# Kernel optimization log

Measured on AMD Instinct MI355X. Metric: run time of the kernel, lower is better.

The kernel has to match this reference:

```python
import jax, jax.numpy as jnp
import numpy as np

TOP_K = 8
NUM_EXPERTS = 256
HIDDEN = 7168
NUM_TOKENS = 16384
NORM_TOPK_PROB = True


def setup_inputs() -> dict:
    key = jax.random.key(0)
    k1, k2 = jax.random.split(key)
    hidden_states = jax.random.normal(k1, (NUM_TOKENS, HIDDEN), dtype=jnp.float32)
    weight = jax.random.normal(k2, (NUM_EXPERTS, HIDDEN), dtype=jnp.float32) * 0.02
    return {"hidden_states": hidden_states, "weight": weight}


def reference(hidden_states, weight):
    # Router logits: [T, E] = [T, H] @ [E, H]^T
    logits = jnp.einsum("th,eh->te", hidden_states, weight)
    # Fused softmax + top-k (npu_moe_gating_top_k_softmax semantics):
    # softmax over experts, then take top-k probabilities and their indices.
    probs = jax.nn.softmax(logits, axis=-1)
    topk_weight, topk_idx = jax.lax.top_k(probs, TOP_K)  # [T, k]
    # row_idx: expert-major (column-major) flattened row indices, as the NPU op returns.
    T = logits.shape[0]
    row_idx = jnp.arange(T * TOP_K, dtype=jnp.int32).reshape(TOP_K, T).T  # [T, k]
    if TOP_K > 1 and NORM_TOPK_PROB:
        denominator = jnp.sum(topk_weight, axis=-1, keepdims=True) + 1e-20
        topk_weight = topk_weight / denominator
    topk_idx = topk_idx.astype(jnp.int32)
    return (topk_idx, topk_weight, row_idx)
```

## Files before the change

kernel.cpp:

```cpp
#include <hip/hip_runtime.h>
#include <hip/hip_bf16.h>

#define NTOK 16384
#define HID 7168
#define NEXP 256
#define TOPK 8

typedef __bf16 bf16x8 __attribute__((ext_vector_type(8)));
typedef float  f32x16 __attribute__((ext_vector_type(16)));

__device__ __align__(16) unsigned short g_wb[NEXP * HID];

__device__ __forceinline__ unsigned int f2bfb(float x) {
    unsigned int u = __float_as_uint(x);
    return (u + 0x7fffu + ((u >> 16) & 1u)) >> 16;
}
__device__ __forceinline__ uint4 pk4(float4 p, float4 q) {
    uint4 u;
    u.x = f2bfb(p.x) | (f2bfb(p.y) << 16);
    u.y = f2bfb(p.z) | (f2bfb(p.w) << 16);
    u.z = f2bfb(q.x) | (f2bfb(q.y) << 16);
    u.w = f2bfb(q.z) | (f2bfb(q.w) << 16);
    return u;
}
__device__ __forceinline__ bf16x8 asbf8(uint4 u) {
    union { uint4 a; bf16x8 b; } c; c.a = u; return c.b;
}

__global__ void wconv_frag(const float* __restrict__ wt) {
    const int tid = blockIdx.x * 256 + threadIdx.x;
    const int l  = tid & 63;
    const int ks = (tid >> 6) & 7;
    const int g  = (tid >> 9) & 7;
    const int p  = tid >> 12;
    const int e  = g * 32 + (l & 31);
    const int kb = p * 128 + ks * 16 + ((l >> 5) << 3);
    const float4* s = (const float4*)(wt + (size_t)e * HID + kb);
    ((uint4*)g_wb)[tid] = pk4(s[0], s[1]);
}

__global__ void moe_rows(float* __restrict__ ob) {
    const int q = blockIdx.x * 256 + threadIdx.x;
    ob[262144 + q] = (float)((q & 7) * NTOK + (q >> 3));
}

__global__ __launch_bounds__(256, 2) void moe_gate_v16(
    const float* __restrict__ hs,
    float* __restrict__ ob)
{
    __shared__ __align__(16) char smem[65536];

    const int tid   = threadIdx.x;
    const int lane  = tid & 63;
    const int w     = tid >> 6;
    const int khalf = lane >> 5;
    const int t0    = blockIdx.x * 32;

    const int srow = tid >> 3;
    const int ssub = tid & 7;
    const char* astage = (const char*)(hs + (size_t)(t0 + srow) * HID + ssub * 8);
    const int stBase = srow * 2048 + ((ssub * 16) ^ ((srow & 7) << 4));

    const int arow  = lane & 31;
    const int abase = arow * 2048;
    const int aswz  = (arow & 7) << 4;

    const char* const bbase = (const char*)g_wb + (size_t)(w * 2) * 8192 + lane * 16;

    f32x16 acc0 = {}, acc1 = {};
    uint4 b0a, b0b, b1a, b1b, b2a, b2b, b3a, b3b;

#define ISSUE_B(SA, SB, J)                                                    \
    do {                                                                      \
        const char* bp = bbase + ((size_t)((J) >> 3) * 64 + ((J) & 7)) * 1024;\
        SA = *(const uint4*)(bp);                                             \
        SB = *(const uint4*)(bp + 8192);                                      \
        __builtin_amdgcn_sched_barrier(0);                                    \
    } while (0)

#define COMPUTE(JL, SA, SB)                                                   \
    do {                                                                      \
        const int off = (((JL) * 32 + khalf * 16) ^ aswz);                    \
        bf16x8 a = *(const bf16x8*)(smem + abase + off);                      \
        acc0 = __builtin_amdgcn_mfma_f32_32x32x16_bf16(a, asbf8(SA), acc0, 0, 0, 0); \
        acc1 = __builtin_amdgcn_mfma_f32_32x32x16_bf16(a, asbf8(SB), acc1, 0, 0, 0); \
    } while (0)

#define VMW(N)                                                                \
    do {                                                                      \
        asm volatile("s_waitcnt vmcnt(" #N ")" ::: "memory");                 \
        __builtin_amdgcn_sched_barrier(0);                                    \
    } while (0)

    for (int c = 0; c < 7; ++c) {
        __syncthreads();
        #pragma unroll
        for (int i = 0; i < 16; ++i) {
            float4 v0 = *(const float4*)(astage + (size_t)c * 4096 + i * 256);
            float4 v1 = *(const float4*)(astage + (size_t)c * 4096 + i * 256 + 16);
            *(uint4*)(smem + stBase + i * 128) = pk4(v0, v1);
        }
        __syncthreads();

        const int C64 = c * 64;
        ISSUE_B(b0a, b0b, C64 + 0);
        ISSUE_B(b1a, b1b, C64 + 1);
        ISSUE_B(b2a, b2b, C64 + 2);
        ISSUE_B(b3a, b3b, C64 + 3);

        for (int jj = 0; jj < 15; ++jj) {
            const int j = jj * 4;
            VMW(6); COMPUTE(j + 0, b0a, b0b); ISSUE_B(b0a, b0b, C64 + j + 4);
            VMW(6); COMPUTE(j + 1, b1a, b1b); ISSUE_B(b1a, b1b, C64 + j + 5);
            VMW(6); COMPUTE(j + 2, b2a, b2b); ISSUE_B(b2a, b2b, C64 + j + 6);
            VMW(6); COMPUTE(j + 3, b3a, b3b); ISSUE_B(b3a, b3b, C64 + j + 7);
        }
        VMW(6); COMPUTE(60, b0a, b0b);
        VMW(4); COMPUTE(61, b1a, b1b);
        VMW(2); COMPUTE(62, b2a, b2b);
        VMW(0); COMPUTE(63, b3a, b3b);
    }

    __syncthreads();

    float* ll = (float*)smem;
    {
        const int ec = w * 64 + (lane & 31);
        #pragma unroll
        for (int r = 0; r < 16; ++r) {
            const int tok = (r & 3) + 8 * (r >> 2) + 4 * khalf;
            ll[tok * 257 + ec]      = acc0[r];
            ll[tok * 257 + ec + 32] = acc1[r];
        }
    }
    __syncthreads();

    if (tid < 32) {
        const float* lr = ll + tid * 257;
        float bv[TOPK]; int bi8[TOPK];
        #pragma unroll
        for (int k = 0; k < TOPK; ++k) { bv[k] = -1e30f; bi8[k] = 0; }
        for (int e = 0; e < NEXP; ++e) {
            const float v = lr[e];
            if (v > bv[TOPK - 1]) {
                int k = TOPK - 1;
                while (k > 0 && v > bv[k - 1]) {
                    bv[k] = bv[k - 1]; bi8[k] = bi8[k - 1]; --k;
                }
                bv[k] = v; bi8[k] = e;
            }
        }
        float ev[TOPK], ssum = 0.f;
        #pragma unroll
        for (int r = 0; r < TOPK; ++r) { ev[r] = expf(bv[r] - bv[0]); ssum += ev[r]; }
        const float inv = 1.0f / ssum;

        const int tg = t0 + tid;
        #pragma unroll
        for (int r = 0; r < TOPK; ++r) {
            ob[(size_t)tg * TOPK + r]          = (float)bi8[r];
            ob[131072 + (size_t)tg * TOPK + r] = ev[r] * inv;
        }
    }
#undef ISSUE_B
#undef COMPUTE
#undef VMW
}

extern "C" void kernel_launch(void* const* d_in, const int* in_sizes, int n_in,
                              void* d_out, int out_size, void* d_ws, size_t ws_size,
                              hipStream_t stream) {
    const float* hs = (const float*)d_in[0];
    const float* wt = (const float*)d_in[1];
    float* ob = (float*)d_out;

    wconv_frag<<<dim3(NEXP * HID / 8 / 256), dim3(256), 0, stream>>>(wt);
    moe_gate_v16<<<dim3(NTOK / 32), dim3(256), 0, stream>>>(hs, ob);
    moe_rows<<<dim3(512), dim3(256), 0, stream>>>(ob);
}
```

Baseline: 245.5 us.

## Split experts across 8 waves, halve K-chunk, stagger chunk order per block

The gating GEMM kernel now uses 512 threads (8 waves), each owning 32 experts with a single accumulator instead of 4 waves with 64 experts each. The K loop stages 512-element chunks (half the shared memory), so more blocks can be resident. It also deepens B prefetch to 8 registers, remaps block IDs to tokens, and rotates each block's starting chunk so concurrent blocks read different weight regions. The intent is better occupancy, latency hiding and spread-out L2/HBM traffic, at the cost of twice as many barrier-separated staging phases.

```diff
diff --git a/kernel.cpp b/kernel.cpp
--- a/kernel.cpp
+++ b/kernel.cpp
@@ -5,6 +5,8 @@
 #define HID 7168
 #define NEXP 256
 #define TOPK 8
+#define NCHK 14
+#define CSTEP 32
 
 typedef __bf16 bf16x8 __attribute__((ext_vector_type(8)));
 typedef float  f32x16 __attribute__((ext_vector_type(16)));
@@ -44,93 +46,100 @@
     ob[262144 + q] = (float)((q & 7) * NTOK + (q >> 3));
 }
 
-__global__ __launch_bounds__(256, 2) void moe_gate_v16(
+__global__ __launch_bounds__(512, 4) void moe_gate_v17(
     const float* __restrict__ hs,
     float* __restrict__ ob)
 {
-    __shared__ __align__(16) char smem[65536];
+    __shared__ __align__(16) char smem[33792];
 
     const int tid   = threadIdx.x;
     const int lane  = tid & 63;
     const int w     = tid >> 6;
     const int khalf = lane >> 5;
-    const int t0    = blockIdx.x * 32;
+    const int bid   = blockIdx.x;
+    const int sb    = (bid & 7) * 64 + (bid >> 3);
+    const int t0    = sb * 32;
+    const int boff  = bid % NCHK;
 
-    const int srow = tid >> 3;
-    const int ssub = tid & 7;
-    const char* astage = (const char*)(hs + (size_t)(t0 + srow) * HID + ssub * 8);
-    const int stBase = srow * 2048 + ((ssub * 16) ^ ((srow & 7) << 4));
+    const int srow = tid >> 4;
+    const int ssub = tid & 15;
+    const float* astage = hs + (size_t)(t0 + srow) * HID + ssub * 32;
+    int adst[4];
+    #pragma unroll
+    for (int d = 0; d < 4; ++d)
+        adst[d] = srow * 1024 + (((ssub * 4 + d) ^ (srow & 7)) << 4);
 
     const int arow  = lane & 31;
-    const int abase = arow * 2048;
-    const int aswz  = (arow & 7) << 4;
+    const int abase = arow * 1024;
+    const int amask = arow & 7;
 
-    const char* const bbase = (const char*)g_wb + (size_t)(w * 2) * 8192 + lane * 16;
+    const char* const bbase = (const char*)g_wb + w * 8192 + lane * 16;
 
-    f32x16 acc0 = {}, acc1 = {};
-    uint4 b0a, b0b, b1a, b1b, b2a, b2b, b3a, b3b;
+    f32x16 acc = {};
+    uint4 b0, b1, b2, b3, b4, b5, b6, b7;
 
-#define ISSUE_B(SA, SB, J)                                                    \
+#define BADDR(J16) (bbase + (size_t)(((J16) >> 3) * 64 + ((J16) & 7)) * 1024)
+#define LOADB(R, J16)                                                         \
+    do { R = *(const uint4*)BADDR(J16); __builtin_amdgcn_sched_barrier(0); } while (0)
+#define CMP(J, R)                                                             \
     do {                                                                      \
-        const char* bp = bbase + ((size_t)((J) >> 3) * 64 + ((J) & 7)) * 1024;\
-        SA = *(const uint4*)(bp);                                             \
-        SB = *(const uint4*)(bp + 8192);                                      \
-        __builtin_amdgcn_sched_barrier(0);                                    \
+        const int off = ((((J) * 2 + khalf) ^ amask) << 4);                   \
+        bf16x8 a = *(const bf16x8*)(smem + abase + off);                      \
+        acc = __builtin_amdgcn_mfma_f32_32x32x16_bf16(a, asbf8(R), acc, 0, 0, 0); \
     } while (0)
-
-#define COMPUTE(JL, SA, SB)                                                   \
-    do {                                                                      \
-        const int off = (((JL) * 32 + khalf * 16) ^ aswz);                    \
-        bf16x8 a = *(const bf16x8*)(smem + abase + off);                      \
-        acc0 = __builtin_amdgcn_mfma_f32_32x32x16_bf16(a, asbf8(SA), acc0, 0, 0, 0); \
-        acc1 = __builtin_amdgcn_mfma_f32_32x32x16_bf16(a, asbf8(SB), acc1, 0, 0, 0); \
-    } while (0)
-
 #define VMW(N)                                                                \
     do {                                                                      \
         asm volatile("s_waitcnt vmcnt(" #N ")" ::: "memory");                 \
         __builtin_amdgcn_sched_barrier(0);                                    \
     } while (0)
 
-    for (int c = 0; c < 7; ++c) {
+    for (int c = 0; c < NCHK; ++c) {
+        int cc = c + boff; if (cc >= NCHK) cc -= NCHK;
+
         __syncthreads();
         #pragma unroll
-        for (int i = 0; i < 16; ++i) {
-            float4 v0 = *(const float4*)(astage + (size_t)c * 4096 + i * 256);
-            float4 v1 = *(const float4*)(astage + (size_t)c * 4096 + i * 256 + 16);
-            *(uint4*)(smem + stBase + i * 128) = pk4(v0, v1);
+        for (int d = 0; d < 4; ++d) {
+            float4 v0 = *(const float4*)(astage + (size_t)cc * 512 + d * 8);
+            float4 v1 = *(const float4*)(astage + (size_t)cc * 512 + d * 8 + 4);
+            *(uint4*)(smem + adst[d]) = pk4(v0, v1);
         }
         __syncthreads();
 
-        const int C64 = c * 64;
-        ISSUE_B(b0a, b0b, C64 + 0);
-        ISSUE_B(b1a, b1b, C64 + 1);
-        ISSUE_B(b2a, b2b, C64 + 2);
-        ISSUE_B(b3a, b3b, C64 + 3);
+        const int J0 = cc * CSTEP;
+        LOADB(b0, J0 + 0); LOADB(b1, J0 + 1); LOADB(b2, J0 + 2); LOADB(b3, J0 + 3);
+        LOADB(b4, J0 + 4); LOADB(b5, J0 + 5); LOADB(b6, J0 + 6); LOADB(b7, J0 + 7);
 
-        for (int jj = 0; jj < 15; ++jj) {
-            const int j = jj * 4;
-            VMW(6); COMPUTE(j + 0, b0a, b0b); ISSUE_B(b0a, b0b, C64 + j + 4);
-            VMW(6); COMPUTE(j + 1, b1a, b1b); ISSUE_B(b1a, b1b, C64 + j + 5);
-            VMW(6); COMPUTE(j + 2, b2a, b2b); ISSUE_B(b2a, b2b, C64 + j + 6);
-            VMW(6); COMPUTE(j + 3, b3a, b3b); ISSUE_B(b3a, b3b, C64 + j + 7);
+        #pragma unroll
+        for (int jj = 0; jj < 3; ++jj) {
+            const int j = jj * 8;
+            VMW(7); CMP(j + 0, b0); LOADB(b0, J0 + j +  8);
+            VMW(7); CMP(j + 1, b1); LOADB(b1, J0 + j +  9);
+            VMW(7); CMP(j + 2, b2); LOADB(b2, J0 + j + 10);
+            VMW(7); CMP(j + 3, b3); LOADB(b3, J0 + j + 11);
+            VMW(7); CMP(j + 4, b4); LOADB(b4, J0 + j + 12);
+            VMW(7); CMP(j + 5, b5); LOADB(b5, J0 + j + 13);
+            VMW(7); CMP(j + 6, b6); LOADB(b6, J0 + j + 14);
+            VMW(7); CMP(j + 7, b7); LOADB(b7, J0 + j + 15);
         }
-        VMW(6); COMPUTE(60, b0a, b0b);
-        VMW(4); COMPUTE(61, b1a, b1b);
-        VMW(2); COMPUTE(62, b2a, b2b);
-        VMW(0); COMPUTE(63, b3a, b3b);
+        VMW(7); CMP(24, b0);
+        VMW(6); CMP(25, b1);
+        VMW(5); CMP(26, b2);
+        VMW(4); CMP(27, b3);
+        VMW(3); CMP(28, b4);
+        VMW(2); CMP(29, b5);
+        VMW(1); CMP(30, b6);
+        VMW(0); CMP(31, b7);
     }
 
     __syncthreads();
 
     float* ll = (float*)smem;
     {
-        const int ec = w * 64 + (lane & 31);
+        const int ec = w * 32 + (lane & 31);
         #pragma unroll
         for (int r = 0; r < 16; ++r) {
             const int tok = (r & 3) + 8 * (r >> 2) + 4 * khalf;
-            ll[tok * 257 + ec]      = acc0[r];
-            ll[tok * 257 + ec + 32] = acc1[r];
+            ll[tok * 257 + ec] = acc[r];
         }
     }
     __syncthreads();
@@ -162,8 +171,9 @@
             ob[131072 + (size_t)tg * TOPK + r] = ev[r] * inv;
         }
     }
-#undef ISSUE_B
-#undef COMPUTE
+#undef BADDR
+#undef LOADB
+#undef CMP
 #undef VMW
 }
 
@@ -175,6 +185,6 @@
     float* ob = (float*)d_out;
 
     wconv_frag<<<dim3(NEXP * HID / 8 / 256), dim3(256), 0, stream>>>(wt);
-    moe_gate_v16<<<dim3(NTOK / 32), dim3(256), 0, stream>>>(hs, ob);
+    moe_gate_v17<<<dim3(NTOK / 32), dim3(512), 0, stream>>>(hs, ob);
     moe_rows<<<dim3(512), dim3(256), 0, stream>>>(ob);
 }
```

After: 264.7 us. 1.08x slower.

## Use 256-token tiles with split-K partials and a separate top-k reduce kernel

Applied to the files above, without the earlier changes.

The gating GEMM now runs as 512-thread blocks that each own 256 tokens and a quarter of the hidden dimension, so there are 64x4 blocks. This replaces 512 blocks of 32 tokens that each streamed the whole bf16 weight matrix. Weight tiles are copied straight into LDS with global_load_lds and double-buffered alongside the converted activation tiles. Each block writes fp32 partial logits to the workspace, and a new reduce kernel sums the splits and does the top-k softmax. This should cut repeated weight traffic from L2 and keep the matrix cores busier, at the cost of extra workspace reads and writes and one more kernel launch.

```diff
diff --git a/kernel.cpp b/kernel.cpp
--- a/kernel.cpp
+++ b/kernel.cpp
@@ -8,6 +8,8 @@
 
 typedef __bf16 bf16x8 __attribute__((ext_vector_type(8)));
 typedef float  f32x16 __attribute__((ext_vector_type(16)));
+typedef __attribute__((address_space(1))) const unsigned char ga_t;
+typedef __attribute__((address_space(3))) unsigned char la_t;
 
 __device__ __align__(16) unsigned short g_wb[NEXP * HID];
 
@@ -23,8 +25,8 @@
     u.w = f2bfb(q.z) | (f2bfb(q.w) << 16);
     return u;
 }
-__device__ __forceinline__ bf16x8 asbf8(uint4 u) {
-    union { uint4 a; bf16x8 b; } c; c.a = u; return c.b;
+__device__ __forceinline__ void gll16(const void* g, void* l) {
+    __builtin_amdgcn_global_load_lds((ga_t*)g, (la_t*)l, 16, 0, 0);
 }
 
 __global__ void wconv_frag(const float* __restrict__ wt) {
@@ -44,98 +46,182 @@
     ob[262144 + q] = (float)((q & 7) * NTOK + (q >> 3));
 }
 
-__global__ __launch_bounds__(256, 2) void moe_gate_v16(
+template<int KS>
+__global__ __launch_bounds__(512, 1) void moe_gate_v19(
     const float* __restrict__ hs,
+    float* __restrict__ pw)
+{
+    constexpr int KLEN  = HID / KS;
+    constexpr int NSTEP = KLEN / 64;
+    __shared__ __align__(16) char smem[131072];
+    char* const bA0 = smem;
+    char* const bA1 = smem + 32768;
+    char* const bB0 = smem + 65536;
+    char* const bB1 = smem + 98304;
+
+    const int tid   = threadIdx.x;
+    const int lane  = tid & 63;
+    const int l31   = lane & 31;
+    const int khalf = lane >> 5;
+    const int wv    = tid >> 6;
+    const int wm    = wv >> 2;
+    const int wn    = wv & 3;
+    const int t0    = blockIdx.x * 256;
+    const int by    = blockIdx.y;
+
+    const int r = tid >> 1;
+    const int h = tid & 1;
+    const float* aptr = hs + (size_t)(t0 + r) * HID + by * KLEN + h * 32;
+    int awb[4];
+    #pragma unroll
+    for (int j = 0; j < 4; ++j)
+        awb[j] = r * 128 + ((h * 64 + j * 16) ^ ((r & 7) << 4));
+
+    const char* const bsrc0 = (const char*)g_wb
+        + ((size_t)by * (KLEN / 128)) * 65536 + wv * 8192 + lane * 16;
+    const int bdst = wv * 4096;
+
+    int arowb[4];
+    #pragma unroll
+    for (int mi = 0; mi < 4; ++mi)
+        arowb[mi] = (wm * 128 + mi * 32 + l31) * 128;
+    int offk[4];
+    #pragma unroll
+    for (int kk = 0; kk < 4; ++kk)
+        offk[kk] = (kk * 32 + khalf * 16) ^ ((l31 & 7) << 4);
+
+    f32x16 acc[4][2] = {};
+    float4 fa[8];
+
+#define LOADA(S)                                                              \
+    do {                                                                      \
+        _Pragma("unroll")                                                     \
+        for (int j = 0; j < 8; ++j)                                           \
+            fa[j] = *(const float4*)(aptr + (size_t)(S) * 64 + j * 4);        \
+        __builtin_amdgcn_sched_barrier(0);                                    \
+    } while (0)
+
+#define ISSUEB(S, BUF)                                                       \
+    do {                                                                      \
+        const char* sp = bsrc0 + ((size_t)((S) >> 1)) * 65536 + ((S) & 1) * 4096; \
+        _Pragma("unroll")                                                     \
+        for (int q = 0; q < 4; ++q)                                           \
+            gll16(sp + q * 1024, (BUF) + bdst + q * 1024);                    \
+        __builtin_amdgcn_sched_barrier(0);                                    \
+    } while (0)
+
+#define CVTWRITE(BUF)                                                        \
+    do {                                                                      \
+        _Pragma("unroll")                                                     \
+        for (int j = 0; j < 4; ++j)                                           \
+            *(uint4*)((BUF) + awb[j]) = pk4(fa[2 * j], fa[2 * j + 1]);        \
+    } while (0)
+
+#define COMPUTE(BA, BB)                                                      \
+    do {                                                                      \
+        _Pragma("unroll")                                                     \
+        for (int kk = 0; kk < 4; ++kk) {                                      \
+            bf16x8 av[4], bv[2];                                              \
+            _Pragma("unroll")                                                 \
+            for (int mi = 0; mi < 4; ++mi)                                    \
+                av[mi] = *(const bf16x8*)((BA) + arowb[mi] + offk[kk]);       \
+            _Pragma("unroll")                                                 \
+            for (int n = 0; n < 2; ++n)                                       \
+                bv[n] = *(const bf16x8*)((BB) + (2 * wn + n) * 4096 + kk * 1024 + lane * 16); \
+            _Pragma("unroll")                                                 \
+            for (int mi = 0; mi < 4; ++mi)                                    \
+                _Pragma("unroll")                                             \
+                for (int n = 0; n < 2; ++n)                                   \
+                    acc[mi][n] = __builtin_amdgcn_mfma_f32_32x32x16_bf16(     \
+                        av[mi], bv[n], acc[mi][n], 0, 0, 0);                  \
+        }                                                                     \
+    } while (0)
+
+#define VMWB(N)                                                              \
+    do {                                                                      \
+        asm volatile("s_waitcnt vmcnt(" #N ")" ::: "memory");                 \
+        __builtin_amdgcn_sched_barrier(0);                                    \
+        asm volatile("s_barrier" ::: "memory");                               \
+        __builtin_amdgcn_sched_barrier(0);                                    \
+    } while (0)
+
+#define LGKB()                                                               \
+    do {                                                                      \
+        asm volatile("s_waitcnt lgkmcnt(0)\n\ts_barrier" ::: "memory");       \
+        __builtin_amdgcn_sched_barrier(0);                                    \
+    } while (0)
+
+    LOADA(0);
+    ISSUEB(0, bB0);
+    CVTWRITE(bA0);
+    LGKB();
+
+    for (int s = 0; s < NSTEP; s += 2) {
+        LOADA(s + 1);
+        ISSUEB(s + 1, bB1);
+        VMWB(12);
+        COMPUTE(bA0, bB0);
+        CVTWRITE(bA1);
+        LGKB();
+
+        if (s + 2 < NSTEP) {
+            LOADA(s + 2);
+            ISSUEB(s + 2, bB0);
+            VMWB(12);
+            COMPUTE(bA1, bB1);
+            CVTWRITE(bA0);
+            LGKB();
+        } else {
+            VMWB(0);
+            COMPUTE(bA1, bB1);
+        }
+    }
+
+    float* const base = pw + ((size_t)by * NTOK + t0) * 256;
+    #pragma unroll
+    for (int mi = 0; mi < 4; ++mi)
+        #pragma unroll
+        for (int n = 0; n < 2; ++n)
+            #pragma unroll
+            for (int rr = 0; rr < 16; ++rr) {
+                const int tokl = wm * 128 + mi * 32 + (rr & 3) + 8 * (rr >> 2) + 4 * khalf;
+                const int ec   = wn * 64 + n * 32 + l31;
+                base[(size_t)tokl * 256 + ec] = acc[mi][n][rr];
+            }
+#undef LOADA
+#undef ISSUEB
+#undef CVTWRITE
+#undef COMPUTE
+#undef VMWB
+#undef LGKB
+}
+
+template<int KS>
+__global__ __launch_bounds__(256) void moe_reduce(
+    const float* __restrict__ pw,
     float* __restrict__ ob)
 {
-    __shared__ __align__(16) char smem[65536];
-
-    const int tid   = threadIdx.x;
-    const int lane  = tid & 63;
-    const int w     = tid >> 6;
-    const int khalf = lane >> 5;
-    const int t0    = blockIdx.x * 32;
-
-    const int srow = tid >> 3;
-    const int ssub = tid & 7;
-    const char* astage = (const char*)(hs + (size_t)(t0 + srow) * HID + ssub * 8);
-    const int stBase = srow * 2048 + ((ssub * 16) ^ ((srow & 7) << 4));
-
-    const int arow  = lane & 31;
-    const int abase = arow * 2048;
-    const int aswz  = (arow & 7) << 4;
-
-    const char* const bbase = (const char*)g_wb + (size_t)(w * 2) * 8192 + lane * 16;
-
-    f32x16 acc0 = {}, acc1 = {};
-    uint4 b0a, b0b, b1a, b1b, b2a, b2b, b3a, b3b;
-
-#define ISSUE_B(SA, SB, J)                                                    \
-    do {                                                                      \
-        const char* bp = bbase + ((size_t)((J) >> 3) * 64 + ((J) & 7)) * 1024;\
-        SA = *(const uint4*)(bp);                                             \
-        SB = *(const uint4*)(bp + 8192);                                      \
-        __builtin_amdgcn_sched_barrier(0);                                    \
-    } while (0)
-
-#define COMPUTE(JL, SA, SB)                                                   \
-    do {                                                                      \
-        const int off = (((JL) * 32 + khalf * 16) ^ aswz);                    \
-        bf16x8 a = *(const bf16x8*)(smem + abase + off);                      \
-        acc0 = __builtin_amdgcn_mfma_f32_32x32x16_bf16(a, asbf8(SA), acc0, 0, 0, 0); \
-        acc1 = __builtin_amdgcn_mfma_f32_32x32x16_bf16(a, asbf8(SB), acc1, 0, 0, 0); \
-    } while (0)
-
-#define VMW(N)                                                                \
-    do {                                                                      \
-        asm volatile("s_waitcnt vmcnt(" #N ")" ::: "memory");                 \
-        __builtin_amdgcn_sched_barrier(0);                                    \
-    } while (0)
-
-    for (int c = 0; c < 7; ++c) {
-        __syncthreads();
-        #pragma unroll
-        for (int i = 0; i < 16; ++i) {
-            float4 v0 = *(const float4*)(astage + (size_t)c * 4096 + i * 256);
-            float4 v1 = *(const float4*)(astage + (size_t)c * 4096 + i * 256 + 16);
-            *(uint4*)(smem + stBase + i * 128) = pk4(v0, v1);
-        }
-        __syncthreads();
-
-        const int C64 = c * 64;
-        ISSUE_B(b0a, b0b, C64 + 0);
-        ISSUE_B(b1a, b1b, C64 + 1);
-        ISSUE_B(b2a, b2b, C64 + 2);
-        ISSUE_B(b3a, b3b, C64 + 3);
-
-        for (int jj = 0; jj < 15; ++jj) {
-            const int j = jj * 4;
-            VMW(6); COMPUTE(j + 0, b0a, b0b); ISSUE_B(b0a, b0b, C64 + j + 4);
-            VMW(6); COMPUTE(j + 1, b1a, b1b); ISSUE_B(b1a, b1b, C64 + j + 5);
-            VMW(6); COMPUTE(j + 2, b2a, b2b); ISSUE_B(b2a, b2b, C64 + j + 6);
-            VMW(6); COMPUTE(j + 3, b3a, b3b); ISSUE_B(b3a, b3b, C64 + j + 7);
-        }
-        VMW(6); COMPUTE(60, b0a, b0b);
-        VMW(4); COMPUTE(61, b1a, b1b);
-        VMW(2); COMPUTE(62, b2a, b2b);
-        VMW(0); COMPUTE(63, b3a, b3b);
-    }
-
+    __shared__ float ll[64 * 257];
+    const int tid = threadIdx.x;
+    const size_t ro = (size_t)blockIdx.x * 16384;
+    const size_t PS = (size_t)NTOK * 256;
+
+    #pragma unroll
+    for (int j = 0; j < 16; ++j) {
+        const size_t f = (size_t)j * 1024 + tid * 4;
+        float4 v = *(const float4*)(pw + ro + f);
+        #pragma unroll
+        for (int s = 1; s < KS; ++s) {
+            float4 u = *(const float4*)(pw + s * PS + ro + f);
+            v.x += u.x; v.y += u.y; v.z += u.z; v.w += u.w;
+        }
+        const int t = (int)(f >> 8);
+        const int e = (int)(f & 255);
+        *(float4*)&ll[t * 257 + e] = v;
+    }
     __syncthreads();
 
-    float* ll = (float*)smem;
-    {
-        const int ec = w * 64 + (lane & 31);
-        #pragma unroll
-        for (int r = 0; r < 16; ++r) {
-            const int tok = (r & 3) + 8 * (r >> 2) + 4 * khalf;
-            ll[tok * 257 + ec]      = acc0[r];
-            ll[tok * 257 + ec + 32] = acc1[r];
-        }
-    }
-    __syncthreads();
-
-    if (tid < 32) {
+    if (tid < 64) {
         const float* lr = ll + tid * 257;
         float bv[TOPK]; int bi8[TOPK];
         #pragma unroll
@@ -152,19 +238,16 @@
         }
         float ev[TOPK], ssum = 0.f;
         #pragma unroll
-        for (int r = 0; r < TOPK; ++r) { ev[r] = expf(bv[r] - bv[0]); ssum += ev[r]; }
+        for (int rr = 0; rr < TOPK; ++rr) { ev[rr] = expf(bv[rr] - bv[0]); ssum += ev[rr]; }
         const float inv = 1.0f / ssum;
 
-        const int tg = t0 + tid;
-        #pragma unroll
-        for (int r = 0; r < TOPK; ++r) {
-            ob[(size_t)tg * TOPK + r]          = (float)bi8[r];
-            ob[131072 + (size_t)tg * TOPK + r] = ev[r] * inv;
-        }
-    }
-#undef ISSUE_B
-#undef COMPUTE
-#undef VMW
+        const int tg = blockIdx.x * 64 + tid;
+        #pragma unroll
+        for (int rr = 0; rr < TOPK; ++rr) {
+            ob[(size_t)tg * TOPK + rr]          = (float)bi8[rr];
+            ob[131072 + (size_t)tg * TOPK + rr] = ev[rr] * inv;
+        }
+    }
 }
 
 extern "C" void kernel_launch(void* const* d_in, const int* in_sizes, int n_in,
@@ -173,8 +256,17 @@
     const float* hs = (const float*)d_in[0];
     const float* wt = (const float*)d_in[1];
     float* ob = (float*)d_out;
+    float* pw = (float*)d_ws;
 
     wconv_frag<<<dim3(NEXP * HID / 8 / 256), dim3(256), 0, stream>>>(wt);
-    moe_gate_v16<<<dim3(NTOK / 32), dim3(256), 0, stream>>>(hs, ob);
+
+    const size_t need4 = (size_t)4 * NTOK * NEXP * sizeof(float);
+    if (ws_size >= need4) {
+        moe_gate_v19<4><<<dim3(64, 4), dim3(512), 0, stream>>>(hs, pw);
+        moe_reduce<4><<<dim3(256), dim3(256), 0, stream>>>(pw, ob);
+    } else {
+        moe_gate_v19<1><<<dim3(64, 1), dim3(512), 0, stream>>>(hs, pw);
+        moe_reduce<1><<<dim3(256), dim3(256), 0, stream>>>(pw, ob);
+    }
     moe_rows<<<dim3(512), dim3(256), 0, stream>>>(ob);
 }
```

After: 416.6 us. 69.7% more time.

## Split GEMM over expert halves and K-splits with separate reduce/top-k kernel

Applied to the files above, without the earlier changes.

Restructures the router GEMM so each block computes 32 tokens × 128 experts over a K slice, with a 2D grid (expert half × K split) and a double-buffered small LDS tile for higher occupancy. Partial logits are written to workspace and a new reduce kernel sums the K-split partials and does top-k/softmax for 64 tokens per block. This trades the extra global round-trip of partial logits and redundant A loads per expert half for more parallelism and latency hiding.

```diff
diff --git a/kernel.cpp b/kernel.cpp
--- a/kernel.cpp
+++ b/kernel.cpp
@@ -44,98 +44,126 @@
     ob[262144 + q] = (float)((q & 7) * NTOK + (q >> 3));
 }
 
-__global__ __launch_bounds__(256, 2) void moe_gate_v16(
+template<int KS>
+__global__ __launch_bounds__(256, 6) void moe_gate_v20(
     const float* __restrict__ hs,
+    float* __restrict__ pw)
+{
+    constexpr int KLEN  = HID / KS;
+    constexpr int NSTEP = KLEN / 64;
+    __shared__ __align__(16) char smem[8192];
+
+    const int tid   = threadIdx.x;
+    const int lane  = tid & 63;
+    const int l31   = lane & 31;
+    const int khalf = lane >> 5;
+    const int w     = tid >> 6;
+    const int t0    = blockIdx.x * 32;
+    const int ez    = blockIdx.y & 1;
+    const int kz    = blockIdx.y >> 1;
+
+    const int ar = tid >> 3;
+    const int akc = tid & 7;
+    const float* aptr = hs + (size_t)(t0 + ar) * HID + kz * KLEN + akc * 8;
+    const int awb = ar * 128 + ((akc ^ (ar & 7)) << 4);
+
+    const int arbase = l31 * 128;
+    const int armask = l31 & 7;
+
+    const char* const bbase = (const char*)g_wb + (ez * 4 + w) * 8192 + lane * 16;
+
+    f32x16 acc = {};
+    float4 fa0, fa1;
+    uint4 b0, b1, b2, b3;
+
+#define LOADA(S)                                                              \
+    do {                                                                      \
+        fa0 = *(const float4*)(aptr + (size_t)(S) * 64);                      \
+        fa1 = *(const float4*)(aptr + (size_t)(S) * 64 + 4);                  \
+    } while (0)
+
+#define WRITEA(BUF)                                                           \
+    do { *(uint4*)((BUF) + awb) = pk4(fa0, fa1); } while (0)
+
+#define LOADB(S)                                                              \
+    do {                                                                      \
+        const char* sp = bbase + (size_t)(kz * (KLEN / 128) + ((S) >> 1)) * 65536 \
+                       + ((S) & 1) * 4096;                                    \
+        b0 = *(const uint4*)(sp);                                             \
+        b1 = *(const uint4*)(sp + 1024);                                      \
+        b2 = *(const uint4*)(sp + 2048);                                      \
+        b3 = *(const uint4*)(sp + 3072);                                      \
+    } while (0)
+
+#define COMPUTE(BUF)                                                          \
+    do {                                                                      \
+        bf16x8 a;                                                             \
+        a = *(const bf16x8*)((BUF) + arbase + (((0 * 2 + khalf) ^ armask) << 4)); \
+        acc = __builtin_amdgcn_mfma_f32_32x32x16_bf16(a, asbf8(b0), acc, 0, 0, 0); \
+        a = *(const bf16x8*)((BUF) + arbase + (((1 * 2 + khalf) ^ armask) << 4)); \
+        acc = __builtin_amdgcn_mfma_f32_32x32x16_bf16(a, asbf8(b1), acc, 0, 0, 0); \
+        a = *(const bf16x8*)((BUF) + arbase + (((2 * 2 + khalf) ^ armask) << 4)); \
+        acc = __builtin_amdgcn_mfma_f32_32x32x16_bf16(a, asbf8(b2), acc, 0, 0, 0); \
+        a = *(const bf16x8*)((BUF) + arbase + (((3 * 2 + khalf) ^ armask) << 4)); \
+        acc = __builtin_amdgcn_mfma_f32_32x32x16_bf16(a, asbf8(b3), acc, 0, 0, 0); \
+    } while (0)
+
+    char* cur = smem;
+    char* oth = smem + 4096;
+
+    LOADA(0); LOADB(0);
+    WRITEA(cur);
+    __syncthreads();
+
+    for (int s = 0; s < NSTEP; ++s) {
+        const bool more = (s + 1 < NSTEP);
+        if (more) LOADA(s + 1);
+        COMPUTE(cur);
+        if (more) {
+            LOADB(s + 1);
+            WRITEA(oth);
+            __syncthreads();
+        }
+        char* t = cur; cur = oth; oth = t;
+    }
+
+    #pragma unroll
+    for (int r = 0; r < 16; ++r) {
+        const int tok = (r & 3) + 8 * (r >> 2) + 4 * khalf;
+        pw[((size_t)kz * NTOK + t0 + tok) * 256 + ez * 128 + w * 32 + l31] = acc[r];
+    }
+#undef LOADA
+#undef WRITEA
+#undef LOADB
+#undef COMPUTE
+}
+
+template<int KS>
+__global__ __launch_bounds__(256) void moe_reduce(
+    const float* __restrict__ pw,
     float* __restrict__ ob)
 {
-    __shared__ __align__(16) char smem[65536];
-
-    const int tid   = threadIdx.x;
-    const int lane  = tid & 63;
-    const int w     = tid >> 6;
-    const int khalf = lane >> 5;
-    const int t0    = blockIdx.x * 32;
-
-    const int srow = tid >> 3;
-    const int ssub = tid & 7;
-    const char* astage = (const char*)(hs + (size_t)(t0 + srow) * HID + ssub * 8);
-    const int stBase = srow * 2048 + ((ssub * 16) ^ ((srow & 7) << 4));
-
-    const int arow  = lane & 31;
-    const int abase = arow * 2048;
-    const int aswz  = (arow & 7) << 4;
-
-    const char* const bbase = (const char*)g_wb + (size_t)(w * 2) * 8192 + lane * 16;
-
-    f32x16 acc0 = {}, acc1 = {};
-    uint4 b0a, b0b, b1a, b1b, b2a, b2b, b3a, b3b;
-
-#define ISSUE_B(SA, SB, J)                                                    \
-    do {                                                                      \
-        const char* bp = bbase + ((size_t)((J) >> 3) * 64 + ((J) & 7)) * 1024;\
-        SA = *(const uint4*)(bp);                                             \
-        SB = *(const uint4*)(bp + 8192);                                      \
-        __builtin_amdgcn_sched_barrier(0);                                    \
-    } while (0)
-
-#define COMPUTE(JL, SA, SB)                                                   \
-    do {                                                                      \
-        const int off = (((JL) * 32 + khalf * 16) ^ aswz);                    \
-        bf16x8 a = *(const bf16x8*)(smem + abase + off);                      \
-        acc0 = __builtin_amdgcn_mfma_f32_32x32x16_bf16(a, asbf8(SA), acc0, 0, 0, 0); \
-        acc1 = __builtin_amdgcn_mfma_f32_32x32x16_bf16(a, asbf8(SB), acc1, 0, 0, 0); \
-    } while (0)
-
-#define VMW(N)                                                                \
-    do {                                                                      \
-        asm volatile("s_waitcnt vmcnt(" #N ")" ::: "memory");                 \
-        __builtin_amdgcn_sched_barrier(0);                                    \
-    } while (0)
-
-    for (int c = 0; c < 7; ++c) {
-        __syncthreads();
-        #pragma unroll
-        for (int i = 0; i < 16; ++i) {
-            float4 v0 = *(const float4*)(astage + (size_t)c * 4096 + i * 256);
-            float4 v1 = *(const float4*)(astage + (size_t)c * 4096 + i * 256 + 16);
-            *(uint4*)(smem + stBase + i * 128) = pk4(v0, v1);
-        }
-        __syncthreads();
-
-        const int C64 = c * 64;
-        ISSUE_B(b0a, b0b, C64 + 0);
-        ISSUE_B(b1a, b1b, C64 + 1);
-        ISSUE_B(b2a, b2b, C64 + 2);
-        ISSUE_B(b3a, b3b, C64 + 3);
-
-        for (int jj = 0; jj < 15; ++jj) {
-            const int j = jj * 4;
-            VMW(6); COMPUTE(j + 0, b0a, b0b); ISSUE_B(b0a, b0b, C64 + j + 4);
-            VMW(6); COMPUTE(j + 1, b1a, b1b); ISSUE_B(b1a, b1b, C64 + j + 5);
-            VMW(6); COMPUTE(j + 2, b2a, b2b); ISSUE_B(b2a, b2b, C64 + j + 6);
-            VMW(6); COMPUTE(j + 3, b3a, b3b); ISSUE_B(b3a, b3b, C64 + j + 7);
-        }
-        VMW(6); COMPUTE(60, b0a, b0b);
-        VMW(4); COMPUTE(61, b1a, b1b);
-        VMW(2); COMPUTE(62, b2a, b2b);
-        VMW(0); COMPUTE(63, b3a, b3b);
-    }
-
+    __shared__ float ll[64 * 257];
+    const int tid = threadIdx.x;
+    const size_t ro = (size_t)blockIdx.x * 16384;
+    const size_t PS = (size_t)NTOK * 256;
+
+    #pragma unroll
+    for (int j = 0; j < 16; ++j) {
+        const size_t f = (size_t)j * 1024 + tid * 4;
+        float4 v = *(const float4*)(pw + ro + f);
+        #pragma unroll
+        for (int s = 1; s < KS; ++s) {
+            float4 u = *(const float4*)(pw + s * PS + ro + f);
+            v.x += u.x; v.y += u.y; v.z += u.z; v.w += u.w;
+        }
+        const int t = (int)(f >> 8);
+        const int e = (int)(f & 255);
+        *(float4*)&ll[t * 257 + e] = v;
+    }
     __syncthreads();
 
-    float* ll = (float*)smem;
-    {
-        const int ec = w * 64 + (lane & 31);
-        #pragma unroll
-        for (int r = 0; r < 16; ++r) {
-            const int tok = (r & 3) + 8 * (r >> 2) + 4 * khalf;
-            ll[tok * 257 + ec]      = acc0[r];
-            ll[tok * 257 + ec + 32] = acc1[r];
-        }
-    }
-    __syncthreads();
-
-    if (tid < 32) {
+    if (tid < 64) {
         const float* lr = ll + tid * 257;
         float bv[TOPK]; int bi8[TOPK];
         #pragma unroll
@@ -152,19 +180,16 @@
         }
         float ev[TOPK], ssum = 0.f;
         #pragma unroll
-        for (int r = 0; r < TOPK; ++r) { ev[r] = expf(bv[r] - bv[0]); ssum += ev[r]; }
+        for (int rr = 0; rr < TOPK; ++rr) { ev[rr] = expf(bv[rr] - bv[0]); ssum += ev[rr]; }
         const float inv = 1.0f / ssum;
 
-        const int tg = t0 + tid;
-        #pragma unroll
-        for (int r = 0; r < TOPK; ++r) {
-            ob[(size_t)tg * TOPK + r]          = (float)bi8[r];
-            ob[131072 + (size_t)tg * TOPK + r] = ev[r] * inv;
-        }
-    }
-#undef ISSUE_B
-#undef COMPUTE
-#undef VMW
+        const int tg = blockIdx.x * 64 + tid;
+        #pragma unroll
+        for (int rr = 0; rr < TOPK; ++rr) {
+            ob[(size_t)tg * TOPK + rr]          = (float)bi8[rr];
+            ob[131072 + (size_t)tg * TOPK + rr] = ev[rr] * inv;
+        }
+    }
 }
 
 extern "C" void kernel_launch(void* const* d_in, const int* in_sizes, int n_in,
@@ -173,8 +198,17 @@
     const float* hs = (const float*)d_in[0];
     const float* wt = (const float*)d_in[1];
     float* ob = (float*)d_out;
+    float* pw = (float*)d_ws;
 
     wconv_frag<<<dim3(NEXP * HID / 8 / 256), dim3(256), 0, stream>>>(wt);
-    moe_gate_v16<<<dim3(NTOK / 32), dim3(256), 0, stream>>>(hs, ob);
+
+    const size_t need2 = (size_t)2 * NTOK * NEXP * sizeof(float);
+    if (ws_size >= need2) {
+        moe_gate_v20<2><<<dim3(512, 4), dim3(256), 0, stream>>>(hs, pw);
+        moe_reduce<2><<<dim3(256), dim3(256), 0, stream>>>(pw, ob);
+    } else {
+        moe_gate_v20<1><<<dim3(512, 2), dim3(256), 0, stream>>>(hs, pw);
+        moe_reduce<1><<<dim3(256), dim3(256), 0, stream>>>(pw, ob);
+    }
     moe_rows<<<dim3(512), dim3(256), 0, stream>>>(ob);
 }
```

Result: slower. 315.3 us (+28.4%).
